# Optimization experiments

Measured on AMD Instinct MI355X. Metric: run time of the kernel, lower is better.

## Reference

```python
import jax, jax.numpy as jnp
import numpy as np

# DSCNPair config (init_kwargs)
C = 256          # d_model
G = 16           # group
K = 3            # kernel_size
DW = 3           # dw_kernel_size
PAD = 1
STRIDE = 1
DIL = 1
GC = C // G      # group_channels
P = K * K        # sampling points per group
OFFSET_SCALE = 1.0
B, H, W = 8, 64, 64


def _dwconv(x, w, b, pad):
    # depthwise conv: x (N,C,H,W), w (C,1,kh,kw)
    out = jax.lax.conv_general_dilated(
        x, w, (1, 1), [(pad, pad), (pad, pad)],
        dimension_numbers=('NCHW', 'OIHW', 'NCHW'), feature_group_count=x.shape[1])
    return out + b[None, :, None, None]


def _dcn_core(x, offset, mask):
    # x: (N,H,W,C) NHWC; offset: (N,H,W,G*P*2); mask: (N,H,W,G*P) already softmaxed per group
    N, Hh, Ww, _ = x.shape
    xp = jnp.pad(x, ((0, 0), (PAD, PAD), (PAD, PAD), (0, 0)))
    Hp, Wp = Hh + 2 * PAD, Ww + 2 * PAD
    Ho = (Hp - (DIL * (K - 1) + 1)) // STRIDE + 1
    Wo = (Wp - (DIL * (K - 1) + 1)) // STRIDE + 1
    # reference points (normalized by padded spatial size)
    base = (DIL * (K - 1)) // 2 + 0.5
    ref_y = (base + jnp.arange(Ho, dtype=x.dtype) * STRIDE) / Hp
    ref_x = (base + jnp.arange(Wo, dtype=x.dtype) * STRIDE) / Wp
    # dilation grid, kw-major ordering to match torch.meshgrid(lin_w, lin_h) in DCNv3
    pts = -((DIL * (K - 1)) // 2) + jnp.arange(K, dtype=x.dtype) * DIL
    gx = jnp.repeat(pts, K) / Wp
    gy = jnp.tile(pts, K) / Hp
    off = offset.reshape(N, Ho, Wo, G, P, 2) * (OFFSET_SCALE / jnp.array([Wp, Hp], x.dtype))
    loc_x = ref_x[None, None, :, None, None] + OFFSET_SCALE * gx + off[..., 0]  # (N,Ho,Wo,G,P)
    loc_y = ref_y[None, :, None, None, None] + OFFSET_SCALE * gy + off[..., 1]
    # grid_sample(bilinear, padding_mode='zeros', align_corners=False):
    # grid g = 2*loc-1; unnormalized idx = ((g+1)*size - 1)/2 = loc*size - 0.5
    ix = loc_x * Wp - 0.5
    iy = loc_y * Hp - 0.5
    x0 = jnp.floor(ix)
    y0 = jnp.floor(iy)
    xg = xp.reshape(N, Hp, Wp, G, GC)
    n_idx = jnp.arange(N)[:, None, None, None, None]
    g_idx = jnp.arange(G)[None, None, None, :, None]

    def gather(yi, xi):
        valid = ((yi >= 0) & (yi < Hp) & (xi >= 0) & (xi < Wp)).astype(x.dtype)
        yc = jnp.clip(yi, 0, Hp - 1).astype(jnp.int32)
        xc = jnp.clip(xi, 0, Wp - 1).astype(jnp.int32)
        return xg[n_idx, yc, xc, g_idx] * valid[..., None]  # (N,Ho,Wo,G,P,GC)

    wx1 = ix - x0; wx0 = 1.0 - wx1
    wy1 = iy - y0; wy0 = 1.0 - wy1
    out = (gather(y0, x0) * (wy0 * wx0)[..., None]
           + gather(y0, x0 + 1) * (wy0 * wx1)[..., None]
           + gather(y0 + 1, x0) * (wy1 * wx0)[..., None]
           + gather(y0 + 1, x0 + 1) * (wy1 * wx1)[..., None])
    out = (out * mask.reshape(N, Ho, Wo, G, P, 1)).sum(4)   # (N,Ho,Wo,G,GC)
    return out.reshape(N, Ho, Wo, G * GC)


def _forward(x, conv0_w, conv0_b, dw_w, dw_b, ln_g, ln_b, off_w, off_b,
             msk_w, msk_b, in_w, in_b, outp_w, outp_b, pw_w, pw_b):
    u = x
    h = _dwconv(x, conv0_w, conv0_b, 2)             # 5x5 depthwise, pad 2
    inp = jnp.transpose(h, (0, 2, 3, 1))            # NHWC, input to DCNv3
    xproj = inp @ in_w + in_b                       # input_proj
    # dw_conv branch: depthwise conv -> LayerNorm(channels_last) -> GELU
    x1 = _dwconv(jnp.transpose(inp, (0, 3, 1, 2)), dw_w, dw_b, (DW - 1) // 2)
    x1 = jnp.transpose(x1, (0, 2, 3, 1))
    mu = x1.mean(-1, keepdims=True)
    var = jnp.mean((x1 - mu) ** 2, -1, keepdims=True)
    x1 = (x1 - mu) * jax.lax.rsqrt(var + 1e-5) * ln_g + ln_b
    x1 = jax.nn.gelu(x1, approximate=False)
    offset = x1 @ off_w + off_b                     # (B,H,W,G*P*2)
    m = jax.nn.softmax((x1 @ msk_w + msk_b).reshape(B, H, W, G, P), axis=-1)
    m = m.reshape(B, H, W, G * P)
    y = _dcn_core(xproj, offset, m)
    y = y @ outp_w + outp_b                         # output_proj
    attn = jnp.einsum('nhwc,dc->ndhw', y, pw_w) + pw_b[None, :, None, None]  # 1x1 conv
    return u * attn


def setup_inputs() -> dict:
    key = jax.random.key(0)
    ks = jax.random.split(key, 8)
    s = 0.05
    return {
        'x': jax.random.normal(ks[0], (B, C, H, W), jnp.float32),
        'conv0_w': jax.random.normal(ks[1], (C, 1, 5, 5), jnp.float32) * s,
        'conv0_b': jnp.zeros((C,), jnp.float32),
        'dw_w': jax.random.normal(ks[2], (C, 1, DW, DW), jnp.float32) * s,
        'dw_b': jnp.zeros((C,), jnp.float32),
        'ln_g': jnp.ones((C,), jnp.float32),
        'ln_b': jnp.zeros((C,), jnp.float32),
        'off_w': jax.random.normal(ks[3], (C, G * P * 2), jnp.float32) * s,
        'off_b': jnp.zeros((G * P * 2,), jnp.float32),
        'msk_w': jax.random.normal(ks[4], (C, G * P), jnp.float32) * s,
        'msk_b': jnp.zeros((G * P,), jnp.float32),
        'in_w': jax.random.normal(ks[5], (C, C), jnp.float32) * s,
        'in_b': jnp.zeros((C,), jnp.float32),
        'outp_w': jax.random.normal(ks[6], (C, C), jnp.float32) * s,
        'outp_b': jnp.zeros((C,), jnp.float32),
        'pw_w': jax.random.normal(ks[7], (C, C), jnp.float32) * s,
        'pw_b': jnp.zeros((C,), jnp.float32),
    }


def reference(x, conv0_w, conv0_b, dw_w, dw_b, ln_g, ln_b, off_w, off_b,
              msk_w, msk_b, in_w, in_b, outp_w, outp_b, pw_w, pw_b):
    return _forward(x, conv0_w, conv0_b, dw_w, dw_b, ln_g, ln_b, off_w, off_b,
                    msk_w, msk_b, in_w, in_b, outp_w, outp_b, pw_w, pw_b)
```

## Files before the change

### kernel.cpp

```cpp
#include <hip/hip_runtime.h>
#include <hip/hip_bf16.h>
#include <hip/hip_fp16.h>
#include <math.h>

#define BB 8
#define CC 256
#define HH 64
#define WW 64
#define GG 16
#define GCH 16
#define PP 9
#define NPIX (BB*HH*WW)

typedef __attribute__((ext_vector_type(4))) float f32x4;
typedef __bf16 bf16x8 __attribute__((ext_vector_type(8)));

#define GLOAD_LDS16(g, l) __builtin_amdgcn_global_load_lds( \
    (const __attribute__((address_space(1))) unsigned int*)(g), \
    (__attribute__((address_space(3))) unsigned int*)(l), 16, 0, 0)

__device__ __forceinline__ void bfu2(unsigned a, float& lo, float& hi) {
    union { unsigned u; float f; } t0, t1;
    t0.u = a << 16; t1.u = a & 0xffff0000u;
    lo = t0.f; hi = t1.f;
}

__global__ void prep_kernel(const float* __restrict__ inw, const float* __restrict__ offw,
                            const float* __restrict__ mskw, const float* __restrict__ outpw,
                            const float* __restrict__ pww, const float* __restrict__ outpb,
                            const float* __restrict__ pwb, const float* __restrict__ offb,
                            const float* __restrict__ mskb,
                            __hip_bfloat16* __restrict__ bt_in, __hip_bfloat16* __restrict__ bt_om,
                            __hip_bfloat16* __restrict__ bt_wc, float* __restrict__ bcomb,
                            float* __restrict__ bcat) {
    __shared__ float pd[256];
    int bid = blockIdx.x;
    int t = threadIdx.x;
    if (bid < 256) {
        bt_in[bid * 256 + t] = __float2bfloat16(inw[t * 256 + bid]);
    } else if (bid < 704) {
        int n = bid - 256;
        float v = 0.0f;
        if (n < 288)      v = offw[t * 288 + n];
        else if (n < 432) v = mskw[t * 144 + (n - 288)];
        bt_om[(size_t)n * 256 + t] = __float2bfloat16(v);
    } else if (bid < 960) {
        int d = bid - 704;
        pd[t] = pww[d * 256 + t];
        __syncthreads();
        const float* ow = outpw + t * 256;
        float s = 0.0f;
        #pragma unroll 8
        for (int c = 0; c < 256; ++c) s += ow[c] * pd[c];
        bt_wc[d * 256 + t] = __float2bfloat16(s);
    } else if (bid == 960) {
        const float* pr = pww + t * 256;
        float s = pwb[t];
        #pragma unroll 8
        for (int c = 0; c < 256; ++c) s += outpb[c] * pr[c];
        bcomb[t] = s;
    } else {
        int i = (bid - 961) * 256 + t;
        if (i < 448) bcat[i] = (i < 288) ? offb[i] : (i < 432 ? mskb[i - 288] : 0.0f);
    }
}

#define C0PLANE 817
__global__ void conv0_kernel(const float* __restrict__ x, const float* __restrict__ w,
                             const float* __restrict__ b,
                             __hip_bfloat16* __restrict__ out_bf) {
    __shared__ float sx[16 * C0PLANE];
    int t  = threadIdx.x;
    int st = blockIdx.x;
    int cg = blockIdx.y;
    int n  = blockIdx.z;
    int h0 = st * 8;
    int c0 = cg * 16;

    #pragma unroll
    for (int i = 0; i < 12; ++i) {
        int task = i * 256 + t;
        int lane = task & 15;
        int pair = task >> 4;
        int c    = pair / 12;
        int row  = pair - c * 12;
        int gy   = h0 - 2 + row;
        float4 v = make_float4(0.f, 0.f, 0.f, 0.f);
        if (gy >= 0 && gy < HH)
            v = *(const float4*)(x + (((size_t)(n * CC + c0 + c)) * HH + gy) * WW + lane * 4);
        *(float4*)&sx[c * C0PLANE + row * 68 + 2 + lane * 4] = v;
    }
    if (t < 192) {
        int c = t / 12, row = t - (t / 12) * 12;
        float* p = &sx[c * C0PLANE + row * 68];
        p[0] = 0.f; p[1] = 0.f; p[66] = 0.f; p[67] = 0.f;
    }
    __syncthreads();

    int c = t & 15;
    int s = t >> 4;
    float wreg[25];
    const float* wp = w + (c0 + c) * 25;
    #pragma unroll
    for (int i = 0; i < 25; ++i) wreg[i] = wp[i];
    float bias = b[c0 + c];
    const float* cp = &sx[c * C0PLANE + s * 4];

    float win[5][8];
    #pragma unroll
    for (int rr = 0; rr < 4; ++rr)
        #pragma unroll
        for (int j = 0; j < 8; ++j) win[rr][j] = cp[rr * 68 + j];

    #pragma unroll
    for (int r = 0; r < 8; ++r) {
        #pragma unroll
        for (int j = 0; j < 8; ++j) win[(r + 4) % 5][j] = cp[(r + 4) * 68 + j];
        float a0 = bias, a1 = bias, a2 = bias, a3 = bias;
        #pragma unroll
        for (int dy = 0; dy < 5; ++dy) {
            const float* wr = &wreg[dy * 5];
            const float* wd = win[(r + dy) % 5];
            #pragma unroll
            for (int dx = 0; dx < 5; ++dx) {
                float wv = wr[dx];
                a0 += wd[0 + dx] * wv;
                a1 += wd[1 + dx] * wv;
                a2 += wd[2 + dx] * wv;
                a3 += wd[3 + dx] * wv;
            }
        }
        size_t pixb = ((size_t)n * 4096 + (h0 + r) * 64 + s * 4) << 8;
        out_bf[pixb + c0 + c]       = __float2bfloat16(a0);
        out_bf[pixb + 256 + c0 + c] = __float2bfloat16(a1);
        out_bf[pixb + 512 + c0 + c] = __float2bfloat16(a2);
        out_bf[pixb + 768 + c0 + c] = __float2bfloat16(a3);
    }
}

__global__ void dwln_kernel(const __hip_bfloat16* __restrict__ inp, const float* __restrict__ dww,
                            const float* __restrict__ dwb, const float* __restrict__ lng,
                            const float* __restrict__ lnb, __hip_bfloat16* __restrict__ x1) {
    __shared__ float sx[3 * 10 * 256];
    __shared__ float ls1[8][4], ls2[8][4];
    int t  = threadIdx.x;
    int x0 = blockIdx.x * 8;
    int h  = blockIdx.y;
    int n  = blockIdx.z;

    #pragma unroll
    for (int i = 0; i < 4; ++i) {
        int task = i * 256 + t;
        if (task < 960) {
            int c8  = task & 31;
            int rem = task >> 5;
            int r   = rem / 10;
            int xx  = rem - r * 10;
            int gy = h + r - 1, gx = x0 + xx - 1;
            float4 A = make_float4(0.f,0.f,0.f,0.f), B = make_float4(0.f,0.f,0.f,0.f);
            if (gy >= 0 && gy < HH && gx >= 0 && gx < WW) {
                uint4 u = *(const uint4*)(inp + (((size_t)(n * HH + gy)) * WW + gx) * CC + c8 * 8);
                bfu2(u.x, A.x, A.y); bfu2(u.y, A.z, A.w);
                bfu2(u.z, B.x, B.y); bfu2(u.w, B.z, B.w);
            }
            *(float4*)&sx[(r * 10 + xx) * 256 + c8 * 8]     = A;
            *(float4*)&sx[(r * 10 + xx) * 256 + c8 * 8 + 4] = B;
        }
    }
    __syncthreads();

    int c = t;
    float wr[9];
    #pragma unroll
    for (int i = 0; i < 9; ++i) wr[i] = dww[c * 9 + i];
    float bias = dwb[c];
    float a[8];
    #pragma unroll
    for (int px = 0; px < 8; ++px) {
        float acc = bias;
        #pragma unroll
        for (int dy = 0; dy < 3; ++dy)
            #pragma unroll
            for (int dx = 0; dx < 3; ++dx)
                acc += sx[(dy * 10 + px + dx) * 256 + c] * wr[dy * 3 + dx];
        a[px] = acc;
    }

    int wid = t >> 6, lane = t & 63;
    #pragma unroll
    for (int px = 0; px < 8; ++px) {
        float s1 = a[px], s2 = a[px] * a[px];
        #pragma unroll
        for (int o = 1; o < 64; o <<= 1) {
            s1 += __shfl_xor(s1, o);
            s2 += __shfl_xor(s2, o);
        }
        if (lane == 0) { ls1[px][wid] = s1; ls2[px][wid] = s2; }
    }
    __syncthreads();

    float gam = lng[c], bet = lnb[c];
    #pragma unroll
    for (int px = 0; px < 8; ++px) {
        float t1 = ls1[px][0] + ls1[px][1] + ls1[px][2] + ls1[px][3];
        float t2 = ls2[px][0] + ls2[px][1] + ls2[px][2] + ls2[px][3];
        float mu  = t1 * (1.0f/256.0f);
        float var = t2 * (1.0f/256.0f) - mu * mu;
        float rr  = rsqrtf(var + 1e-5f);
        float v = (a[px] - mu) * rr * gam + bet;
        float g = 0.5f * v * (1.0f + erff(v * 0.70710678118654752440f));
        x1[(((size_t)(n * HH + h)) * WW + x0 + px) * CC + c] = __float2bfloat16(g);
    }
}

__device__ __forceinline__ void stage_tile(const __hip_bfloat16* __restrict__ A,
                                           const __hip_bfloat16* __restrict__ Bt,
                                           __bf16* As, __bf16* Bs,
                                           int bm, int bn, int k0, int w, int l) {
    #pragma unroll
    for (int i = 0; i < 4; ++i) {
        int q = w*256 + i*64 + l;
        int row = q >> 3, sk = q & 7;
        const __hip_bfloat16* g = A + (((size_t)(bm + row)) << 8) + k0 + sk*8;
        GLOAD_LDS16(g, As + (w*256 + i*64)*8);
    }
    #pragma unroll
    for (int i = 0; i < 2; ++i) {
        int q = w*128 + i*64 + l;
        int row = q >> 3, sk = q & 7;
        const __hip_bfloat16* g = Bt + (((size_t)(bn + row)) << 8) + k0 + sk*8;
        GLOAD_LDS16(g, Bs + (w*128 + i*64)*8);
    }
}

__global__ void mgemm_kernel(const __hip_bfloat16* __restrict__ A,
                             const __hip_bfloat16* __restrict__ Bt,
                             const float* __restrict__ bias,
                             __hip_bfloat16* __restrict__ Cout, int ldc) {
    __shared__ __bf16 smem[24576];
    int tid = threadIdx.x;
    int w = tid >> 6, l = tid & 63;
    int bn = blockIdx.x * 64;
    int bm = blockIdx.y * 128;
    __bf16* Asb[2] = { smem,        smem + 12288 };
    __bf16* Bsb[2] = { smem + 8192, smem + 20480 };
    f32x4 acc[2][4];
    #pragma unroll
    for (int m = 0; m < 2; ++m)
        #pragma unroll
        for (int n = 0; n < 4; ++n)
            acc[m][n] = (f32x4){0.f, 0.f, 0.f, 0.f};

    stage_tile(A, Bt, Asb[0], Bsb[0], bm, bn, 0, w, l);
    __syncthreads();
    int lr = l & 15, kg = l >> 4;
    #pragma unroll
    for (int t = 0; t < 4; ++t) {
        int cur = t & 1;
        if (t < 3) stage_tile(A, Bt, Asb[cur^1], Bsb[cur^1], bm, bn, (t+1)*64, w, l);
        const __bf16* Ab = Asb[cur];
        const __bf16* Bb = Bsb[cur];
        bf16x8 af[2][2], bfr[4][2];
        #pragma unroll
        for (int m = 0; m < 2; ++m)
            #pragma unroll
            for (int u = 0; u < 2; ++u)
                af[m][u] = *(const bf16x8*)&Ab[(w*32 + m*16 + lr)*64 + u*32 + kg*8];
        #pragma unroll
        for (int n = 0; n < 4; ++n)
            #pragma unroll
            for (int u = 0; u < 2; ++u)
                bfr[n][u] = *(const bf16x8*)&Bb[(n*16 + lr)*64 + u*32 + kg*8];
        #pragma unroll
        for (int u = 0; u < 2; ++u)
            #pragma unroll
            for (int m = 0; m < 2; ++m)
                #pragma unroll
                for (int n = 0; n < 4; ++n)
                    acc[m][n] = __builtin_amdgcn_mfma_f32_16x16x32_bf16(af[m][u], bfr[n][u], acc[m][n], 0, 0, 0);
        __syncthreads();
    }
    int orow = bm + w*32 + kg*4;
    #pragma unroll
    for (int n = 0; n < 4; ++n) {
        int ccol = bn + n*16 + lr;
        float bv = bias[ccol];
        #pragma unroll
        for (int m = 0; m < 2; ++m) {
            #pragma unroll
            for (int j = 0; j < 4; ++j) {
                size_t o = (size_t)(orow + m*16 + j) * ldc + ccol;
                Cout[o] = __float2bfloat16(acc[m][n][j] + bv);
            }
        }
    }
}

__global__ void omgemm_kernel(const __hip_bfloat16* __restrict__ A,
                              const __hip_bfloat16* __restrict__ Bt,
                              const float* __restrict__ bias,
                              __hip_bfloat16* __restrict__ off_bf,
                              __hip_bfloat16* __restrict__ msk_bf) {
    __shared__ __bf16 smem[24576];
    int tid = threadIdx.x;
    int w = tid >> 6, l = tid & 63;
    int bn = blockIdx.x * 64;
    int bm = blockIdx.y * 128;
    __bf16* Asb[2] = { smem,        smem + 12288 };
    __bf16* Bsb[2] = { smem + 8192, smem + 20480 };
    f32x4 acc[2][4];
    #pragma unroll
    for (int m = 0; m < 2; ++m)
        #pragma unroll
        for (int n = 0; n < 4; ++n)
            acc[m][n] = (f32x4){0.f, 0.f, 0.f, 0.f};

    stage_tile(A, Bt, Asb[0], Bsb[0], bm, bn, 0, w, l);
    __syncthreads();
    int lr = l & 15, kg = l >> 4;
    #pragma unroll
    for (int t = 0; t < 4; ++t) {
        int cur = t & 1;
        if (t < 3) stage_tile(A, Bt, Asb[cur^1], Bsb[cur^1], bm, bn, (t+1)*64, w, l);
        const __bf16* Ab = Asb[cur];
        const __bf16* Bb = Bsb[cur];
        bf16x8 af[2][2], bfr[4][2];
        #pragma unroll
        for (int m = 0; m < 2; ++m)
            #pragma unroll
            for (int u = 0; u < 2; ++u)
                af[m][u] = *(const bf16x8*)&Ab[(w*32 + m*16 + lr)*64 + u*32 + kg*8];
        #pragma unroll
        for (int n = 0; n < 4; ++n)
            #pragma unroll
            for (int u = 0; u < 2; ++u)
                bfr[n][u] = *(const bf16x8*)&Bb[(n*16 + lr)*64 + u*32 + kg*8];
        #pragma unroll
        for (int u = 0; u < 2; ++u)
            #pragma unroll
            for (int m = 0; m < 2; ++m)
                #pragma unroll
                for (int n = 0; n < 4; ++n)
                    acc[m][n] = __builtin_amdgcn_mfma_f32_16x16x32_bf16(af[m][u], bfr[n][u], acc[m][n], 0, 0, 0);
        __syncthreads();
    }
    int orow = bm + w*32 + kg*4;
    #pragma unroll
    for (int n = 0; n < 4; ++n) {
        int ccol = bn + n*16 + lr;
        if (ccol >= 432) continue;
        float bv = bias[ccol];
        #pragma unroll
        for (int m = 0; m < 2; ++m) {
            #pragma unroll
            for (int j = 0; j < 4; ++j) {
                int row = orow + m*16 + j;
                float v = acc[m][n][j] + bv;
                if (ccol < 288)
                    off_bf[(size_t)row * 288 + ccol] = __float2bfloat16(v);
                else
                    msk_bf[(size_t)row * 144 + (ccol - 288)] = __float2bfloat16(v);
            }
        }
    }
}

__global__ void attn_fused_kernel(const __hip_bfloat16* __restrict__ A,
                                  const __hip_bfloat16* __restrict__ Bt,
                                  const float* __restrict__ bias,
                                  const float* __restrict__ x,
                                  float* __restrict__ out) {
    __shared__ __bf16 smem[24576];
    int tid = threadIdx.x;
    int w = tid >> 6, l = tid & 63;
    int bn = blockIdx.x * 64;
    int bm = blockIdx.y * 128;
    __bf16* Asb[2] = { smem,        smem + 12288 };
    __bf16* Bsb[2] = { smem + 8192, smem + 20480 };
    f32x4 acc[2][4];
    #pragma unroll
    for (int m = 0; m < 2; ++m)
        #pragma unroll
        for (int n = 0; n < 4; ++n)
            acc[m][n] = (f32x4){0.f, 0.f, 0.f, 0.f};

    stage_tile(A, Bt, Asb[0], Bsb[0], bm, bn, 0, w, l);
    __syncthreads();
    int lr = l & 15, kg = l >> 4;
    #pragma unroll
    for (int t = 0; t < 4; ++t) {
        int cur = t & 1;
        if (t < 3) stage_tile(A, Bt, Asb[cur^1], Bsb[cur^1], bm, bn, (t+1)*64, w, l);
        const __bf16* Ab = Asb[cur];
        const __bf16* Bb = Bsb[cur];
        bf16x8 af[2][2], bfr[4][2];
        #pragma unroll
        for (int m = 0; m < 2; ++m)
            #pragma unroll
            for (int u = 0; u < 2; ++u)
                af[m][u] = *(const bf16x8*)&Ab[(w*32 + m*16 + lr)*64 + u*32 + kg*8];
        #pragma unroll
        for (int n = 0; n < 4; ++n)
            #pragma unroll
            for (int u = 0; u < 2; ++u)
                bfr[n][u] = *(const bf16x8*)&Bb[(n*16 + lr)*64 + u*32 + kg*8];
        #pragma unroll
        for (int u = 0; u < 2; ++u)
            #pragma unroll
            for (int m = 0; m < 2; ++m)
                #pragma unroll
                for (int n = 0; n < 4; ++n)
                    acc[m][n] = __builtin_amdgcn_mfma_f32_16x16x32_bf16(af[m][u], bfr[n][u], acc[m][n], 0, 0, 0);
        __syncthreads();
    }

    float* cLds = (float*)smem;
    int rel0 = w*32 + kg*4;
    #pragma unroll
    for (int n = 0; n < 4; ++n) {
        int col = n*16 + lr;
        float bv = bias[bn + col];
        #pragma unroll
        for (int m = 0; m < 2; ++m) {
            #pragma unroll
            for (int j = 0; j < 4; ++j)
                cLds[col * 133 + rel0 + m*16 + j] = acc[m][n][j] + bv;
        }
    }
    __syncthreads();

    int d  = tid >> 2;
    int po = (tid & 3) * 32;
    int n_img = bm >> 12;
    int rem   = bm & 4095;
    size_t gb = (((size_t)(n_img * CC + bn + d)) << 12) + rem + po;
    const float* xr = x + gb;
    float* ow = out + gb;
    const float* cr = &cLds[d * 133 + po];
    #pragma unroll
    for (int j = 0; j < 32; j += 4) {
        float4 xv = *(const float4*)(xr + j);
        float4 r;
        r.x = xv.x * cr[j+0];
        r.y = xv.y * cr[j+1];
        r.z = xv.z * cr[j+2];
        r.w = xv.w * cr[j+3];
        *(float4*)(ow + j) = r;
    }
}

__global__ void dcn_kernel(const __hip_bfloat16* __restrict__ xproj,
                           const __hip_bfloat16* __restrict__ off,
                           const __hip_bfloat16* __restrict__ mlog,
                           __hip_bfloat16* __restrict__ y) {
    __shared__ uint2 wLds[1152];
    __shared__ int   oLds[1152];
    int bid = blockIdx.x;
    int blk = (bid & 7) * 512 + (bid >> 3);
    int pix0 = blk * 8;
    int t = threadIdx.x;

    if (t < 128) {
        int px = t >> 4;
        int g  = t & 15;
        int pix = pix0 + px;
        int wo = pix & 63, ho = (pix >> 6) & 63;
        const __hip_bfloat16* mb = mlog + (size_t)pix * 144 + g * 9;
        float lg[9];
        float mx = -1e30f;
        #pragma unroll
        for (int p = 0; p < 9; ++p) { lg[p] = __bfloat162float(mb[p]); mx = fmaxf(mx, lg[p]); }
        float se = 0.f;
        #pragma unroll
        for (int p = 0; p < 9; ++p) { lg[p] = __expf(lg[p] - mx); se += lg[p]; }
        float rs = 1.0f / se;
        const unsigned* ob = (const unsigned*)(off + (size_t)pix * 288 + g * 18);
        #pragma unroll
        for (int p = 0; p < 9; ++p) {
            float ox, oy;
            bfu2(ob[p], ox, oy);
            float m = lg[p] * rs;
            int dx = p / 3 - 1;
            int dy = p - (p / 3) * 3 - 1;
            float fx = (float)(wo + dx) + ox;
            float fy = (float)(ho + dy) + oy;
            float x0f = floorf(fx), y0f = floorf(fy);
            int x0 = (int)x0f, y0 = (int)y0f;
            int x1 = x0 + 1, y1 = y0 + 1;
            float wx1 = fx - x0f, wx0 = 1.0f - wx1;
            float wy1 = fy - y0f, wy0 = 1.0f - wy1;
            float vx0 = (x0 >= 0 && x0 < WW) ? 1.0f : 0.0f;
            float vx1 = (x1 >= 0 && x1 < WW) ? 1.0f : 0.0f;
            float vy0 = (y0 >= 0 && y0 < HH) ? 1.0f : 0.0f;
            float vy1 = (y1 >= 0 && y1 < HH) ? 1.0f : 0.0f;
            int x0c = min(max(x0, 0), WW - 1), x1c = min(max(x1, 0), WW - 1);
            int y0c = min(max(y0, 0), HH - 1), y1c = min(max(y1, 0), HH - 1);
            int tau = px * 144 + g * 9 + p;
            union { __half2 h2; unsigned u; } pa, pb;
            pa.h2 = __floats2half2_rn(m * wy0 * wx0 * vy0 * vx0,
                                      m * wy0 * wx1 * vy0 * vx1);
            pb.h2 = __floats2half2_rn(m * wy1 * wx0 * vy1 * vx0,
                                      m * wy1 * wx1 * vy1 * vx1);
            wLds[tau] = make_uint2(pa.u, pb.u);
            oLds[tau] = (y0c * WW + x0c) | ((x1c - x0c) << 12) | ((y1c - y0c) << 13);
        }
    }
    __syncthreads();

    int px = t >> 5;
    int l  = t & 31;
    int g  = l >> 1;
    int ch = g * 16 + (l & 1) * 8;
    int pix = pix0 + px;
    int n = pix >> 12;
    const __hip_bfloat16* xb = xproj + ((size_t)n << 20) + ch;
    float a0=0,a1=0,a2=0,a3=0,a4=0,a5=0,a6=0,a7=0;
    const uint2* wp = &wLds[px * 144 + g * 9];
    const int*   op = &oLds[px * 144 + g * 9];
    #pragma unroll
    for (int p = 0; p < 9; ++p) {
        uint2 pw = wp[p];
        union { unsigned u; __half2 h2; } ua, ub;
        ua.u = pw.x; ub.u = pw.y;
        float2 fA = __half22float2(ua.h2);
        float2 fB = __half22float2(ub.h2);
        float w00 = fA.x, w01 = fA.y, w10 = fB.x, w11 = fB.y;
        int pk = op[p];
        int base = (pk & 4095) << 8;
        int ddx  = ((pk >> 12) & 1) << 8;
        int ddy  = ((pk >> 13) & 1) << 14;
        {
            uint4 u = *(const uint4*)(xb + base);
            float b0,b1,b2,b3,b4,b5,b6,b7;
            bfu2(u.x,b0,b1); bfu2(u.y,b2,b3); bfu2(u.z,b4,b5); bfu2(u.w,b6,b7);
            a0 += w00*b0; a1 += w00*b1; a2 += w00*b2; a3 += w00*b3;
            a4 += w00*b4; a5 += w00*b5; a6 += w00*b6; a7 += w00*b7;
        }
        {
            uint4 u = *(const uint4*)(xb + base + ddx);
            float b0,b1,b2,b3,b4,b5,b6,b7;
            bfu2(u.x,b0,b1); bfu2(u.y,b2,b3); bfu2(u.z,b4,b5); bfu2(u.w,b6,b7);
            a0 += w01*b0; a1 += w01*b1; a2 += w01*b2; a3 += w01*b3;
            a4 += w01*b4; a5 += w01*b5; a6 += w01*b6; a7 += w01*b7;
        }
        {
            uint4 u = *(const uint4*)(xb + base + ddy);
            float b0,b1,b2,b3,b4,b5,b6,b7;
            bfu2(u.x,b0,b1); bfu2(u.y,b2,b3); bfu2(u.z,b4,b5); bfu2(u.w,b6,b7);
            a0 += w10*b0; a1 += w10*b1; a2 += w10*b2; a3 += w10*b3;
            a4 += w10*b4; a5 += w10*b5; a6 += w10*b6; a7 += w10*b7;
        }
        {
            uint4 u = *(const uint4*)(xb + base + ddy + ddx);
            float b0,b1,b2,b3,b4,b5,b6,b7;
            bfu2(u.x,b0,b1); bfu2(u.y,b2,b3); bfu2(u.z,b4,b5); bfu2(u.w,b6,b7);
            a0 += w11*b0; a1 += w11*b1; a2 += w11*b2; a3 += w11*b3;
            a4 += w11*b4; a5 += w11*b5; a6 += w11*b6; a7 += w11*b7;
        }
    }
    union { __hip_bfloat16 h[8]; uint4 u; } ov;
    ov.h[0]=__float2bfloat16(a0); ov.h[1]=__float2bfloat16(a1);
    ov.h[2]=__float2bfloat16(a2); ov.h[3]=__float2bfloat16(a3);
    ov.h[4]=__float2bfloat16(a4); ov.h[5]=__float2bfloat16(a5);
    ov.h[6]=__float2bfloat16(a6); ov.h[7]=__float2bfloat16(a7);
    *(uint4*)(y + (size_t)pix * CC + ch) = ov.u;
}

extern "C" void kernel_launch(void* const* d_in, const int* in_sizes, int n_in,
                              void* d_out, int out_size, void* d_ws, size_t ws_size,
                              hipStream_t stream) {
    const float* x      = (const float*)d_in[0];
    const float* conv0w = (const float*)d_in[1];
    const float* conv0b = (const float*)d_in[2];
    const float* dww    = (const float*)d_in[3];
    const float* dwb    = (const float*)d_in[4];
    const float* lng    = (const float*)d_in[5];
    const float* lnb    = (const float*)d_in[6];
    const float* offw   = (const float*)d_in[7];
    const float* offb   = (const float*)d_in[8];
    const float* mskw   = (const float*)d_in[9];
    const float* mskb   = (const float*)d_in[10];
    const float* inw    = (const float*)d_in[11];
    const float* inb    = (const float*)d_in[12];
    const float* outpw  = (const float*)d_in[13];
    const float* outpb  = (const float*)d_in[14];
    const float* pww    = (const float*)d_in[15];
    const float* pwb    = (const float*)d_in[16];

    __hip_bfloat16* bfb = (__hip_bfloat16*)d_ws;
    __hip_bfloat16* inp_bf  = bfb;
    __hip_bfloat16* y_bf    = inp_bf;
    __hip_bfloat16* x1_bf   = bfb + 8388608;
    __hip_bfloat16* xpj_bf  = x1_bf;
    __hip_bfloat16* off_bf  = bfb + 16777216;
    __hip_bfloat16* msk_bf  = bfb + 26214400;
    __hip_bfloat16* bt_in   = bfb + 30932992;
    __hip_bfloat16* bt_om   = bt_in + 65536;
    __hip_bfloat16* bt_wc   = bt_om + 114688;
    float* bcomb = (float*)(bt_wc + 65536);
    float* bcat  = bcomb + 256;
    float* out = (float*)d_out;

    prep_kernel<<<963, 256, 0, stream>>>(inw, offw, mskw, outpw, pww, outpb, pwb,
                                         offb, mskb, bt_in, bt_om, bt_wc, bcomb, bcat);
    conv0_kernel<<<dim3(8, 16, BB), 256, 0, stream>>>(x, conv0w, conv0b, inp_bf);
    dwln_kernel<<<dim3(8, 64, BB), 256, 0, stream>>>(inp_bf, dww, dwb, lng, lnb, x1_bf);
    omgemm_kernel<<<dim3(7, 256), 256, 0, stream>>>(x1_bf, bt_om, bcat, off_bf, msk_bf);
    mgemm_kernel<<<dim3(4, 256), 256, 0, stream>>>(inp_bf, bt_in, inb, xpj_bf, 256);
    dcn_kernel<<<NPIX/8, 256, 0, stream>>>(xpj_bf, off_bf, msk_bf, y_bf);
    attn_fused_kernel<<<dim3(4, 256), 256, 0, stream>>>(y_bf, bt_wc, bcomb, x, out);
}
```

Before: 170.0 us.

## Restructure DCN sampling to one thread per pixel-group without LDS staging

```diff
diff --git a/kernel.cpp b/kernel.cpp
--- a/kernel.cpp
+++ b/kernel.cpp
@@ -13,6 +13,7 @@
 #define NPIX (BB*HH*WW)
 
 typedef __attribute__((ext_vector_type(4))) float f32x4;
+typedef __attribute__((ext_vector_type(2))) float f32x2;
 typedef __bf16 bf16x8 __attribute__((ext_vector_type(8)));
 
 #define GLOAD_LDS16(g, l) __builtin_amdgcn_global_load_lds( \
@@ -23,6 +24,11 @@
     union { unsigned u; float f; } t0, t1;
     t0.u = a << 16; t1.u = a & 0xffff0000u;
     lo = t0.f; hi = t1.f;
+}
+__device__ __forceinline__ f32x2 bfup2(unsigned a) {
+    union { unsigned u; float f; } t0, t1;
+    t0.u = a << 16; t1.u = a & 0xffff0000u;
+    return (f32x2){t0.f, t1.f};
 }
 
 __global__ void prep_kernel(const float* __restrict__ inw, const float* __restrict__ offw,
@@ -453,117 +459,100 @@
                            const __hip_bfloat16* __restrict__ off,
                            const __hip_bfloat16* __restrict__ mlog,
                            __hip_bfloat16* __restrict__ y) {
-    __shared__ uint2 wLds[1152];
-    __shared__ int   oLds[1152];
     int bid = blockIdx.x;
-    int blk = (bid & 7) * 512 + (bid >> 3);
-    int pix0 = blk * 8;
-    int t = threadIdx.x;
-
-    if (t < 128) {
-        int px = t >> 4;
-        int g  = t & 15;
-        int pix = pix0 + px;
-        int wo = pix & 63, ho = (pix >> 6) & 63;
-        const __hip_bfloat16* mb = mlog + (size_t)pix * 144 + g * 9;
-        float lg[9];
-        float mx = -1e30f;
-        #pragma unroll
-        for (int p = 0; p < 9; ++p) { lg[p] = __bfloat162float(mb[p]); mx = fmaxf(mx, lg[p]); }
-        float se = 0.f;
-        #pragma unroll
-        for (int p = 0; p < 9; ++p) { lg[p] = __expf(lg[p] - mx); se += lg[p]; }
-        float rs = 1.0f / se;
-        const unsigned* ob = (const unsigned*)(off + (size_t)pix * 288 + g * 18);
-        #pragma unroll
-        for (int p = 0; p < 9; ++p) {
-            float ox, oy;
-            bfu2(ob[p], ox, oy);
-            float m = lg[p] * rs;
-            int dx = p / 3 - 1;
-            int dy = p - (p / 3) * 3 - 1;
-            float fx = (float)(wo + dx) + ox;
-            float fy = (float)(ho + dy) + oy;
-            float x0f = floorf(fx), y0f = floorf(fy);
-            int x0 = (int)x0f, y0 = (int)y0f;
-            int x1 = x0 + 1, y1 = y0 + 1;
-            float wx1 = fx - x0f, wx0 = 1.0f - wx1;
-            float wy1 = fy - y0f, wy0 = 1.0f - wy1;
-            float vx0 = (x0 >= 0 && x0 < WW) ? 1.0f : 0.0f;
-            float vx1 = (x1 >= 0 && x1 < WW) ? 1.0f : 0.0f;
-            float vy0 = (y0 >= 0 && y0 < HH) ? 1.0f : 0.0f;
-            float vy1 = (y1 >= 0 && y1 < HH) ? 1.0f : 0.0f;
-            int x0c = min(max(x0, 0), WW - 1), x1c = min(max(x1, 0), WW - 1);
-            int y0c = min(max(y0, 0), HH - 1), y1c = min(max(y1, 0), HH - 1);
-            int tau = px * 144 + g * 9 + p;
-            union { __half2 h2; unsigned u; } pa, pb;
-            pa.h2 = __floats2half2_rn(m * wy0 * wx0 * vy0 * vx0,
-                                      m * wy0 * wx1 * vy0 * vx1);
-            pb.h2 = __floats2half2_rn(m * wy1 * wx0 * vy1 * vx0,
-                                      m * wy1 * wx1 * vy1 * vx1);
-            wLds[tau] = make_uint2(pa.u, pb.u);
-            oLds[tau] = (y0c * WW + x0c) | ((x1c - x0c) << 12) | ((y1c - y0c) << 13);
-        }
-    }
-    __syncthreads();
-
-    int px = t >> 5;
-    int l  = t & 31;
-    int g  = l >> 1;
-    int ch = g * 16 + (l & 1) * 8;
-    int pix = pix0 + px;
-    int n = pix >> 12;
-    const __hip_bfloat16* xb = xproj + ((size_t)n << 20) + ch;
-    float a0=0,a1=0,a2=0,a3=0,a4=0,a5=0,a6=0,a7=0;
-    const uint2* wp = &wLds[px * 144 + g * 9];
-    const int*   op = &oLds[px * 144 + g * 9];
+    int blk = (bid & 7) * 256 + (bid >> 3);
+    int task = blk * 256 + threadIdx.x;
+    int g   = task & 15;
+    int pix = task >> 4;
+    int wo = pix & 63, ho = (pix >> 6) & 63;
+    int n  = pix >> 12;
+
+    const unsigned* ob = (const unsigned*)(off + (size_t)pix * 288 + g * 18);
+    unsigned opk[9];
+    #pragma unroll
+    for (int p = 0; p < 9; ++p) opk[p] = ob[p];
+    const __hip_bfloat16* mb = mlog + (size_t)pix * 144 + g * 9;
+    float lg[9];
+    float mx = -1e30f;
+    #pragma unroll
+    for (int p = 0; p < 9; ++p) { lg[p] = __bfloat162float(mb[p]); mx = fmaxf(mx, lg[p]); }
+    float se = 0.f;
+    #pragma unroll
+    for (int p = 0; p < 9; ++p) { lg[p] = __expf(lg[p] - mx); se += lg[p]; }
+    float rs = 1.0f / se;
+
+    const __hip_bfloat16* xb = xproj + ((size_t)n << 20) + g * 16;
+    f32x2 A[8];
+    #pragma unroll
+    for (int i = 0; i < 8; ++i) A[i] = (f32x2){0.f, 0.f};
+
     #pragma unroll
     for (int p = 0; p < 9; ++p) {
-        uint2 pw = wp[p];
-        union { unsigned u; __half2 h2; } ua, ub;
-        ua.u = pw.x; ub.u = pw.y;
-        float2 fA = __half22float2(ua.h2);
-        float2 fB = __half22float2(ub.h2);
-        float w00 = fA.x, w01 = fA.y, w10 = fB.x, w11 = fB.y;
-        int pk = op[p];
-        int base = (pk & 4095) << 8;
-        int ddx  = ((pk >> 12) & 1) << 8;
-        int ddy  = ((pk >> 13) & 1) << 14;
-        {
-            uint4 u = *(const uint4*)(xb + base);
-            float b0,b1,b2,b3,b4,b5,b6,b7;
-            bfu2(u.x,b0,b1); bfu2(u.y,b2,b3); bfu2(u.z,b4,b5); bfu2(u.w,b6,b7);
-            a0 += w00*b0; a1 += w00*b1; a2 += w00*b2; a3 += w00*b3;
-            a4 += w00*b4; a5 += w00*b5; a6 += w00*b6; a7 += w00*b7;
-        }
-        {
-            uint4 u = *(const uint4*)(xb + base + ddx);
-            float b0,b1,b2,b3,b4,b5,b6,b7;
-            bfu2(u.x,b0,b1); bfu2(u.y,b2,b3); bfu2(u.z,b4,b5); bfu2(u.w,b6,b7);
-            a0 += w01*b0; a1 += w01*b1; a2 += w01*b2; a3 += w01*b3;
-            a4 += w01*b4; a5 += w01*b5; a6 += w01*b6; a7 += w01*b7;
-        }
-        {
-            uint4 u = *(const uint4*)(xb + base + ddy);
-            float b0,b1,b2,b3,b4,b5,b6,b7;
-            bfu2(u.x,b0,b1); bfu2(u.y,b2,b3); bfu2(u.z,b4,b5); bfu2(u.w,b6,b7);
-            a0 += w10*b0; a1 += w10*b1; a2 += w10*b2; a3 += w10*b3;
-            a4 += w10*b4; a5 += w10*b5; a6 += w10*b6; a7 += w10*b7;
-        }
-        {
-            uint4 u = *(const uint4*)(xb + base + ddy + ddx);
-            float b0,b1,b2,b3,b4,b5,b6,b7;
-            bfu2(u.x,b0,b1); bfu2(u.y,b2,b3); bfu2(u.z,b4,b5); bfu2(u.w,b6,b7);
-            a0 += w11*b0; a1 += w11*b1; a2 += w11*b2; a3 += w11*b3;
-            a4 += w11*b4; a5 += w11*b5; a6 += w11*b6; a7 += w11*b7;
-        }
-    }
-    union { __hip_bfloat16 h[8]; uint4 u; } ov;
-    ov.h[0]=__float2bfloat16(a0); ov.h[1]=__float2bfloat16(a1);
-    ov.h[2]=__float2bfloat16(a2); ov.h[3]=__float2bfloat16(a3);
-    ov.h[4]=__float2bfloat16(a4); ov.h[5]=__float2bfloat16(a5);
-    ov.h[6]=__float2bfloat16(a6); ov.h[7]=__float2bfloat16(a7);
-    *(uint4*)(y + (size_t)pix * CC + ch) = ov.u;
+        float ox, oy;
+        bfu2(opk[p], ox, oy);
+        float m = lg[p] * rs;
+        int dx = p / 3 - 1;
+        int dy = p - (p / 3) * 3 - 1;
+        float fx = (float)(wo + dx) + ox;
+        float fy = (float)(ho + dy) + oy;
+        float x0f = floorf(fx), y0f = floorf(fy);
+        int x0 = (int)x0f, y0 = (int)y0f;
+        int x1 = x0 + 1, y1 = y0 + 1;
+        float wx1 = fx - x0f, wx0 = 1.0f - wx1;
+        float wy1 = fy - y0f, wy0 = 1.0f - wy1;
+        float vx0 = (x0 >= 0 && x0 < WW) ? 1.0f : 0.0f;
+        float vx1 = (x1 >= 0 && x1 < WW) ? 1.0f : 0.0f;
+        float vy0 = (y0 >= 0 && y0 < HH) ? 1.0f : 0.0f;
+        float vy1 = (y1 >= 0 && y1 < HH) ? 1.0f : 0.0f;
+        int x0c = min(max(x0, 0), WW - 1), x1c = min(max(x1, 0), WW - 1);
+        int y0c = min(max(y0, 0), HH - 1), y1c = min(max(y1, 0), HH - 1);
+        float w00 = m * wy0 * wx0 * vy0 * vx0;
+        float w01 = m * wy0 * wx1 * vy0 * vx1;
+        float w10 = m * wy1 * wx0 * vy1 * vx0;
+        float w11 = m * wy1 * wx1 * vy1 * vx1;
+        int base = (y0c * WW + x0c) << 8;
+        int ddx  = (x1c - x0c) << 8;
+        int ddy  = (y1c - y0c) << 14;
+        const __hip_bfloat16* c00 = xb + base;
+        const __hip_bfloat16* c01 = xb + base + ddx;
+        const __hip_bfloat16* c10 = xb + base + ddy;
+        const __hip_bfloat16* c11 = xb + base + ddy + ddx;
+        uint4 uA0 = *(const uint4*)c00,  uA1 = *(const uint4*)(c00 + 8);
+        uint4 uB0 = *(const uint4*)c01,  uB1 = *(const uint4*)(c01 + 8);
+        uint4 uC0 = *(const uint4*)c10,  uC1 = *(const uint4*)(c10 + 8);
+        uint4 uD0 = *(const uint4*)c11,  uD1 = *(const uint4*)(c11 + 8);
+        f32x2 wv;
+        wv = (f32x2){w00, w00};
+        A[0] += wv * bfup2(uA0.x); A[1] += wv * bfup2(uA0.y);
+        A[2] += wv * bfup2(uA0.z); A[3] += wv * bfup2(uA0.w);
+        A[4] += wv * bfup2(uA1.x); A[5] += wv * bfup2(uA1.y);
+        A[6] += wv * bfup2(uA1.z); A[7] += wv * bfup2(uA1.w);
+        wv = (f32x2){w01, w01};
+        A[0] += wv * bfup2(uB0.x); A[1] += wv * bfup2(uB0.y);
+        A[2] += wv * bfup2(uB0.z); A[3] += wv * bfup2(uB0.w);
+        A[4] += wv * bfup2(uB1.x); A[5] += wv * bfup2(uB1.y);
+        A[6] += wv * bfup2(uB1.z); A[7] += wv * bfup2(uB1.w);
+        wv = (f32x2){w10, w10};
+        A[0] += wv * bfup2(uC0.x); A[1] += wv * bfup2(uC0.y);
+        A[2] += wv * bfup2(uC0.z); A[3] += wv * bfup2(uC0.w);
+        A[4] += wv * bfup2(uC1.x); A[5] += wv * bfup2(uC1.y);
+        A[6] += wv * bfup2(uC1.z); A[7] += wv * bfup2(uC1.w);
+        wv = (f32x2){w11, w11};
+        A[0] += wv * bfup2(uD0.x); A[1] += wv * bfup2(uD0.y);
+        A[2] += wv * bfup2(uD0.z); A[3] += wv * bfup2(uD0.w);
+        A[4] += wv * bfup2(uD1.x); A[5] += wv * bfup2(uD1.y);
+        A[6] += wv * bfup2(uD1.z); A[7] += wv * bfup2(uD1.w);
+    }
+
+    union { __hip_bfloat16 h[16]; uint4 u[2]; } ov;
+    #pragma unroll
+    for (int i = 0; i < 8; ++i) {
+        ov.h[2*i]   = __float2bfloat16(A[i].x);
+        ov.h[2*i+1] = __float2bfloat16(A[i].y);
+    }
+    __hip_bfloat16* yp = y + (size_t)pix * CC + g * 16;
+    *(uint4*)yp       = ov.u[0];
+    *(uint4*)(yp + 8) = ov.u[1];
 }
 
 extern "C" void kernel_launch(void* const* d_in, const int* in_sizes, int n_in,
@@ -607,6 +596,6 @@
     dwln_kernel<<<dim3(8, 64, BB), 256, 0, stream>>>(inp_bf, dww, dwb, lng, lnb, x1_bf);
     omgemm_kernel<<<dim3(7, 256), 256, 0, stream>>>(x1_bf, bt_om, bcat, off_bf, msk_bf);
     mgemm_kernel<<<dim3(4, 256), 256, 0, stream>>>(inp_bf, bt_in, inb, xpj_bf, 256);
-    dcn_kernel<<<NPIX/8, 256, 0, stream>>>(xpj_bf, off_bf, msk_bf, y_bf);
+    dcn_kernel<<<2048, 256, 0, stream>>>(xpj_bf, off_bf, msk_bf, y_bf);
     attn_fused_kernel<<<dim3(4, 256), 256, 0, stream>>>(y_bf, bt_wc, bcomb, x, out);
 }
```

After: 200.6 us. +18.0%, slower.
